# Kernel tuning notes

Hardware: AMD Instinct MI355X
Metric: run time of the kernel (lower is better)

Reference implementation:

```python
import jax, jax.numpy as jnp
import numpy as np

B, S, D, H = 4, 2048, 1024, 16
DK = D // H
NEG = -1e9


def setup_inputs() -> dict:
    key = jax.random.key(0)
    k1, k2, k3, k4 = jax.random.split(key, 4)
    x = jax.random.normal(k1, (B, S, D), dtype=jnp.float32)
    # seq_lens sorted descending; first entry must equal max_len (as the torch
    # code uses seq_lens[0] as max_len for the mask)
    sl = jax.random.randint(k2, (B,), S // 2, S + 1)
    sl = jnp.sort(sl)[::-1].at[0].set(S).astype(jnp.int64)
    # params of the output projection nn.Linear(d_m, d_m)
    lim = 1.0 / np.sqrt(D)
    W = jax.random.uniform(k3, (D, D), minval=-lim, maxval=lim, dtype=jnp.float32)
    b = jax.random.uniform(k4, (D,), minval=-lim, maxval=lim, dtype=jnp.float32)
    return {"x": x, "seq_lens": sl, "W": W, "b": b}


def reference(x, seq_lens, W, b):
    # key padding mask: (B, 1, 1, S) -> True where key position is valid
    valid = jnp.arange(S)[None, :] < seq_lens[:, None]          # (B, S)
    mask = valid[:, None, None, :]                              # (B, 1, 1, S)
    # split heads: (B, S, D) -> (B, H, S, DK)
    xh = x.reshape(B, S, H, DK).transpose(0, 2, 1, 3)
    scores = jnp.einsum("bhqd,bhkd->bhqk", xh, xh) / jnp.sqrt(jnp.float32(DK))
    scores = jnp.where(mask, scores, NEG)
    attn = jax.nn.softmax(scores, axis=-1)                      # (B, H, S, S)
    # dropout(0.1) omitted (eval-mode deterministic reference)
    ctx = jnp.einsum("bhqk,bhkd->bhqd", attn, xh)
    ctx = ctx.transpose(0, 2, 1, 3).reshape(B, S, D)
    out = ctx @ W.T + b                                         # (B, S, D)
    return (jnp.sum(out, axis=1), attn)
```

## Files before the change

### kernel.cpp

```cpp
#include <hip/hip_runtime.h>

#define S_  2048
#define D_  1024
#define H_  16
#define B_  4

typedef __attribute__((ext_vector_type(8))) short short8;
typedef __attribute__((ext_vector_type(4))) float f32x4;

__device__ __forceinline__ unsigned short f2bf(float f) {
  unsigned int u = __float_as_uint(f);
  u += 0x7fffu + ((u >> 16) & 1u);
  return (unsigned short)(u >> 16);
}
__device__ __forceinline__ unsigned int pack2(float a, float b) {
  return (unsigned int)f2bf(a) | ((unsigned int)f2bf(b) << 16);
}
__device__ __forceinline__ float h2f(unsigned int u, int shft) {
  unsigned short hs = (unsigned short)(u >> shft);
  return (float)__builtin_bit_cast(_Float16, hs);
}

#define SCL   0.18033688011112042f
#define EBIAS 12.0f

__global__ __launch_bounds__(256) void xcvt(const float* __restrict__ x,
                                            unsigned short* __restrict__ xh) {
  const int n = blockIdx.x;
  const int bh = n >> 5, chunk = n & 31;
  const int b = bh >> 4, h = bh & 15;
  const int r = threadIdx.x >> 2, cg = threadIdx.x & 3;
  const int srow = chunk * 64 + r;
  const float* src = x + ((size_t)b * S_ + srow) * D_ + h * 64 + cg * 16;
  float4 v0 = ((const float4*)src)[0];
  float4 v1 = ((const float4*)src)[1];
  float4 v2 = ((const float4*)src)[2];
  float4 v3 = ((const float4*)src)[3];
  uint4 w0, w1;
  w0.x = pack2(v0.x, v0.y); w0.y = pack2(v0.z, v0.w);
  w0.z = pack2(v1.x, v1.y); w0.w = pack2(v1.z, v1.w);
  w1.x = pack2(v2.x, v2.y); w1.y = pack2(v2.z, v2.w);
  w1.z = pack2(v3.x, v3.y); w1.w = pack2(v3.z, v3.w);
  unsigned short* dst = xh + ((size_t)bh * S_ + srow) * 64 + cg * 16;
  *(uint4*)dst = w0;
  *(uint4*)(dst + 8) = w1;
}

__global__ __launch_bounds__(256, 2) void attn_fused(
    const unsigned short* __restrict__ xh, const int* __restrict__ sl32,
    float* __restrict__ attn, unsigned int* __restrict__ cpart)
{
  __shared__ __align__(16) unsigned short kbuf[64 * 64];
  __shared__ __align__(16) unsigned int ebuf[8][2048];
  __shared__ float wbuf[4][16];
  __shared__ float invbuf[16];

  const int n    = blockIdx.x;
  const int xcd  = n & 7;
  const int slot = n >> 3;
  const int bh   = (slot >> 7) * 8 + xcd;
  const int qt   = slot & 127;
  const int b    = bh >> 4;
  const int tid  = threadIdx.x;
  const int wv   = tid >> 6;
  const int lane = tid & 63;
  const int lo   = lane & 15;
  const int g    = lane >> 4;

  const bool is64 = (sl32[1] == 0);
  const int seqlen = is64 ? sl32[2 * b] : sl32[b];

  const unsigned short* xk = xh + (size_t)bh * S_ * 64;

  short8 aq0 = *(const short8*)(xk + (size_t)(qt * 16 + lo) * 64 + g * 8);
  short8 aq1 = *(const short8*)(xk + (size_t)(qt * 16 + lo) * 64 + g * 8 + 32);

  const int sr = tid >> 2, up = tid & 3;
  uint4 pf0, pf1;
  auto prefetch = [&](int c) {
    const uint4* src = (const uint4*)(xk + (size_t)(c * 64 + sr) * 64) + up * 2;
    pf0 = src[0]; pf1 = src[1];
  };
  auto commit = [&]() {
    uint4* d = (uint4*)&kbuf[sr * 64];
    const int sw = sr & 7;
    d[(up * 2) ^ sw]     = pf0;
    d[(up * 2 + 1) ^ sw] = pf1;
  };

  float rsum[4] = {0.f, 0.f, 0.f, 0.f};
  prefetch(0);
  commit();
  __syncthreads();
  const int lk = wv * 16 + lo;
  const int cs = g ^ (lk & 7);
  const int sA = ((g * 2) & 6) << 2;
  for (int c = 0; c < 32; ++c) {
    if (c < 31) prefetch(c + 1);
    short8 b0 = *(const short8*)&kbuf[lk * 64 + cs * 8];
    short8 b1 = *(const short8*)&kbuf[lk * 64 + (cs ^ 4) * 8];
    f32x4 acc = {0.f, 0.f, 0.f, 0.f};
    acc = __builtin_amdgcn_mfma_f32_16x16x32_bf16(aq0, b0, acc, 0, 0, 0);
    acc = __builtin_amdgcn_mfma_f32_16x16x32_bf16(aq1, b1, acc, 0, 0, 0);
    const int kg = c * 64 + lk;
    const bool valid = kg < seqlen;
    float e0 = valid ? exp2f(acc[0] * SCL - EBIAS) : 0.f;
    float e1 = valid ? exp2f(acc[1] * SCL - EBIAS) : 0.f;
    float e2 = valid ? exp2f(acc[2] * SCL - EBIAS) : 0.f;
    float e3 = valid ? exp2f(acc[3] * SCL - EBIAS) : 0.f;
    rsum[0] += e0; rsum[1] += e1; rsum[2] += e2; rsum[3] += e3;
    ebuf[g * 2][kg ^ sA] =
        __builtin_bit_cast(unsigned int, __builtin_amdgcn_cvt_pkrtz(e0, e1));
    ebuf[g * 2 + 1][kg ^ sA] =
        __builtin_bit_cast(unsigned int, __builtin_amdgcn_cvt_pkrtz(e2, e3));
    __syncthreads();
    if (c < 31) commit();
    __syncthreads();
  }

#pragma unroll
  for (int r = 0; r < 4; ++r) {
    float v = rsum[r];
    v += __shfl_xor(v, 1);
    v += __shfl_xor(v, 2);
    v += __shfl_xor(v, 4);
    v += __shfl_xor(v, 8);
    if (lo == 0) wbuf[wv][g * 4 + r] = v;
  }
  __syncthreads();
  if (tid < 16)
    invbuf[tid] = 1.0f / (wbuf[0][tid] + wbuf[1][tid] + wbuf[2][tid] + wbuf[3][tid]);
  __syncthreads();

  const int wr = tid >> 4, wc = tid & 15;
  const int r2w = wr >> 1, shw = (wr & 1) * 16, sw2 = (r2w & 6) << 2;
  const float vr = invbuf[wr];
  float* prow = attn + (size_t)bh * S_ * S_ + (size_t)(qt * 16 + wr) * S_;
#pragma unroll 8
  for (int i = 0; i < 32; ++i) {
    const int k0 = wc * 4 + i * 64;
    uint4 u = *(const uint4*)&ebuf[r2w][k0 ^ sw2];
    f32x4 v = {h2f(u.x, shw) * vr, h2f(u.y, shw) * vr,
               h2f(u.z, shw) * vr, h2f(u.w, shw) * vr};
    __builtin_nontemporal_store(v, (f32x4*)(prow + k0));
  }

  const int c0 = tid * 8;
  float a0 = 0.f, a1 = 0.f, a2 = 0.f, a3 = 0.f;
  float a4 = 0.f, a5 = 0.f, a6 = 0.f, a7 = 0.f;
#pragma unroll
  for (int r2 = 0; r2 < 8; ++r2) {
    const int s = (r2 & 6) << 2;
    const uint4 uA = *(const uint4*)&ebuf[r2][c0 ^ s];
    const uint4 uB = *(const uint4*)&ebuf[r2][(c0 ^ s) + 4];
    const float i0 = invbuf[2 * r2], i1 = invbuf[2 * r2 + 1];
    a0 += h2f(uA.x, 0) * i0 + h2f(uA.x, 16) * i1;
    a1 += h2f(uA.y, 0) * i0 + h2f(uA.y, 16) * i1;
    a2 += h2f(uA.z, 0) * i0 + h2f(uA.z, 16) * i1;
    a3 += h2f(uA.w, 0) * i0 + h2f(uA.w, 16) * i1;
    a4 += h2f(uB.x, 0) * i0 + h2f(uB.x, 16) * i1;
    a5 += h2f(uB.y, 0) * i0 + h2f(uB.y, 16) * i1;
    a6 += h2f(uB.z, 0) * i0 + h2f(uB.z, 16) * i1;
    a7 += h2f(uB.w, 0) * i0 + h2f(uB.w, 16) * i1;
  }
  uint4 w;
  w.x = __builtin_bit_cast(unsigned int, __builtin_amdgcn_cvt_pkrtz(a0, a1));
  w.y = __builtin_bit_cast(unsigned int, __builtin_amdgcn_cvt_pkrtz(a2, a3));
  w.z = __builtin_bit_cast(unsigned int, __builtin_amdgcn_cvt_pkrtz(a4, a5));
  w.w = __builtin_bit_cast(unsigned int, __builtin_amdgcn_cvt_pkrtz(a6, a7));
  *(uint4*)&cpart[(size_t)(bh * 128 + qt) * 1024 + tid * 4] = w;
}

__global__ __launch_bounds__(256) void creduce(const unsigned int* __restrict__ cpart,
                                               float* __restrict__ c) {
  const int i = blockIdx.x * 256 + threadIdx.x;
  const int bh = i >> 11, k = i & 2047;
  const unsigned short* cp = (const unsigned short*)cpart + (size_t)bh * 128 * 2048 + k;
  float s = 0.f;
#pragma unroll 8
  for (int qt = 0; qt < 128; ++qt)
    s += (float)__builtin_bit_cast(_Float16, cp[(size_t)qt * 2048]);
  c[i] = s;
}

__global__ __launch_bounds__(256) void csum_k(const float* __restrict__ c,
                                              const unsigned short* __restrict__ xh,
                                              float* __restrict__ csump) {
  __shared__ float part[4][64];
  const int bh = blockIdx.x >> 3, oct = blockIdx.x & 7;
  const int seg = threadIdx.x >> 6, d = threadIdx.x & 63;
  const float* cb = c + bh * 2048;
  const unsigned short* xb = xh + (size_t)bh * S_ * 64 + d;
  const int k0 = oct * 256 + seg * 64;
  float acc = 0.f;
#pragma unroll 4
  for (int k = k0; k < k0 + 64; ++k) {
    float xv = __uint_as_float((unsigned int)xb[(size_t)k * 64] << 16);
    acc += cb[k] * xv;
  }
  part[seg][d] = acc;
  __syncthreads();
  if (threadIdx.x < 64)
    csump[((size_t)oct * 64 + bh) * 64 + d] =
        part[0][d] + part[1][d] + part[2][d] + part[3][d];
}

__global__ __launch_bounds__(256) void proj_k(const float* __restrict__ csump,
                                              const float* __restrict__ W,
                                              const float* __restrict__ bias,
                                              float* __restrict__ out0) {
  const int idx = blockIdx.x * 4 + (threadIdx.x >> 6);
  const int b = idx >> 10, d = idx & 1023;
  const int lane = threadIdx.x & 63;
  const float* wr = W + (size_t)d * D_;
  float acc = 0.f;
#pragma unroll
  for (int e = 0; e < 16; ++e) {
    const int ei = lane + e * 64;
    const int bhh = b * 16 + (ei >> 6);
    const int dd = ei & 63;
    float cv = 0.f;
#pragma unroll
    for (int oct = 0; oct < 8; ++oct)
      cv += csump[((size_t)oct * 64 + bhh) * 64 + dd];
    acc += cv * wr[ei];
  }
  acc += __shfl_xor(acc, 32);
  acc += __shfl_xor(acc, 16);
  acc += __shfl_xor(acc, 8);
  acc += __shfl_xor(acc, 4);
  acc += __shfl_xor(acc, 2);
  acc += __shfl_xor(acc, 1);
  if (lane == 0) out0[idx] = acc + 2048.0f * bias[d];
}

extern "C" void kernel_launch(void* const* d_in, const int* in_sizes, int n_in,
                              void* d_out, int out_size, void* d_ws, size_t ws_size,
                              hipStream_t stream) {
  const float* x    = (const float*)d_in[0];
  const int*   sl   = (const int*)d_in[1];
  const float* W    = (const float*)d_in[2];
  const float* bias = (const float*)d_in[3];

  float* out0 = (float*)d_out;
  float* attn = out0 + B_ * D_;

  unsigned int* cpart = (unsigned int*)d_ws;
  float* c     = (float*)(cpart + (size_t)64 * 128 * 1024);
  float* csump = c + 64 * 2048;
  unsigned short* xh = (unsigned short*)(csump + 8 * 64 * 64);

  hipLaunchKernelGGL(xcvt,       dim3(2048), dim3(256), 0, stream, x, xh);
  hipLaunchKernelGGL(attn_fused, dim3(8192), dim3(256), 0, stream, xh, sl, attn, cpart);
  hipLaunchKernelGGL(creduce,    dim3(512),  dim3(256), 0, stream, cpart, c);
  hipLaunchKernelGGL(csum_k,     dim3(512),  dim3(256), 0, stream, c, xh, csump);
  hipLaunchKernelGGL(proj_k,     dim3(1024), dim3(256), 0, stream, csump, W, bias, out0);
}
```

Baseline: 322.2 us.

## Double-buffer K tile to drop a barrier and fuse creduce into csum kernel

```diff
diff --git a/kernel.cpp b/kernel.cpp
--- a/kernel.cpp
+++ b/kernel.cpp
@@ -50,10 +50,10 @@
     const unsigned short* __restrict__ xh, const int* __restrict__ sl32,
     float* __restrict__ attn, unsigned int* __restrict__ cpart)
 {
-  __shared__ __align__(16) unsigned short kbuf[64 * 64];
+  __shared__ __align__(16) unsigned short kbuf[2][64 * 64];
   __shared__ __align__(16) unsigned int ebuf[8][2048];
-  __shared__ float wbuf[4][16];
-  __shared__ float invbuf[16];
+  float* wbuf   = (float*)&kbuf[0][0];
+  float* invbuf = (float*)&kbuf[1][0];
 
   const int n    = blockIdx.x;
   const int xcd  = n & 7;
@@ -81,8 +81,8 @@
     const uint4* src = (const uint4*)(xk + (size_t)(c * 64 + sr) * 64) + up * 2;
     pf0 = src[0]; pf1 = src[1];
   };
-  auto commit = [&]() {
-    uint4* d = (uint4*)&kbuf[sr * 64];
+  auto commit = [&](unsigned short* dst) {
+    uint4* d = (uint4*)&dst[sr * 64];
     const int sw = sr & 7;
     d[(up * 2) ^ sw]     = pf0;
     d[(up * 2 + 1) ^ sw] = pf1;
@@ -90,15 +90,16 @@
 
   float rsum[4] = {0.f, 0.f, 0.f, 0.f};
   prefetch(0);
-  commit();
+  commit(kbuf[0]);
   __syncthreads();
   const int lk = wv * 16 + lo;
   const int cs = g ^ (lk & 7);
   const int sA = ((g * 2) & 6) << 2;
   for (int c = 0; c < 32; ++c) {
     if (c < 31) prefetch(c + 1);
-    short8 b0 = *(const short8*)&kbuf[lk * 64 + cs * 8];
-    short8 b1 = *(const short8*)&kbuf[lk * 64 + (cs ^ 4) * 8];
+    const unsigned short* kb = kbuf[c & 1];
+    short8 b0 = *(const short8*)&kb[lk * 64 + cs * 8];
+    short8 b1 = *(const short8*)&kb[lk * 64 + (cs ^ 4) * 8];
     f32x4 acc = {0.f, 0.f, 0.f, 0.f};
     acc = __builtin_amdgcn_mfma_f32_16x16x32_bf16(aq0, b0, acc, 0, 0, 0);
     acc = __builtin_amdgcn_mfma_f32_16x16x32_bf16(aq1, b1, acc, 0, 0, 0);
@@ -113,8 +114,7 @@
         __builtin_bit_cast(unsigned int, __builtin_amdgcn_cvt_pkrtz(e0, e1));
     ebuf[g * 2 + 1][kg ^ sA] =
         __builtin_bit_cast(unsigned int, __builtin_amdgcn_cvt_pkrtz(e2, e3));
-    __syncthreads();
-    if (c < 31) commit();
+    if (c < 31) commit(kbuf[(c + 1) & 1]);
     __syncthreads();
   }
 
@@ -125,11 +125,11 @@
     v += __shfl_xor(v, 2);
     v += __shfl_xor(v, 4);
     v += __shfl_xor(v, 8);
-    if (lo == 0) wbuf[wv][g * 4 + r] = v;
+    if (lo == 0) wbuf[wv * 16 + g * 4 + r] = v;
   }
   __syncthreads();
   if (tid < 16)
-    invbuf[tid] = 1.0f / (wbuf[0][tid] + wbuf[1][tid] + wbuf[2][tid] + wbuf[3][tid]);
+    invbuf[tid] = 1.0f / (wbuf[tid] + wbuf[16 + tid] + wbuf[32 + tid] + wbuf[48 + tid]);
   __syncthreads();
 
   const int wr = tid >> 4, wc = tid & 15;
@@ -171,36 +171,36 @@
   *(uint4*)&cpart[(size_t)(bh * 128 + qt) * 1024 + tid * 4] = w;
 }
 
-__global__ __launch_bounds__(256) void creduce(const unsigned int* __restrict__ cpart,
-                                               float* __restrict__ c) {
-  const int i = blockIdx.x * 256 + threadIdx.x;
-  const int bh = i >> 11, k = i & 2047;
-  const unsigned short* cp = (const unsigned short*)cpart + (size_t)bh * 128 * 2048 + k;
-  float s = 0.f;
-#pragma unroll 8
-  for (int qt = 0; qt < 128; ++qt)
-    s += (float)__builtin_bit_cast(_Float16, cp[(size_t)qt * 2048]);
-  c[i] = s;
-}
-
-__global__ __launch_bounds__(256) void csum_k(const float* __restrict__ c,
-                                              const unsigned short* __restrict__ xh,
-                                              float* __restrict__ csump) {
+__global__ __launch_bounds__(256) void csum2(const unsigned int* __restrict__ cpart,
+                                             const unsigned short* __restrict__ xh,
+                                             float* __restrict__ csump) {
+  __shared__ float csh[256];
   __shared__ float part[4][64];
   const int bh = blockIdx.x >> 3, oct = blockIdx.x & 7;
-  const int seg = threadIdx.x >> 6, d = threadIdx.x & 63;
-  const float* cb = c + bh * 2048;
+  const int t = threadIdx.x;
+  {
+    const int k = oct * 256 + t;
+    const unsigned short* cp =
+        (const unsigned short*)cpart + (size_t)bh * 128 * 2048 + k;
+    float s = 0.f;
+#pragma unroll 8
+    for (int q = 0; q < 128; ++q)
+      s += (float)__builtin_bit_cast(_Float16, cp[(size_t)q * 2048]);
+    csh[t] = s;
+  }
+  __syncthreads();
+  const int seg = t >> 6, d = t & 63;
   const unsigned short* xb = xh + (size_t)bh * S_ * 64 + d;
   const int k0 = oct * 256 + seg * 64;
   float acc = 0.f;
 #pragma unroll 4
-  for (int k = k0; k < k0 + 64; ++k) {
-    float xv = __uint_as_float((unsigned int)xb[(size_t)k * 64] << 16);
-    acc += cb[k] * xv;
+  for (int kk = 0; kk < 64; ++kk) {
+    float xv = __uint_as_float((unsigned int)xb[(size_t)(k0 + kk) * 64] << 16);
+    acc += csh[seg * 64 + kk] * xv;
   }
   part[seg][d] = acc;
   __syncthreads();
-  if (threadIdx.x < 64)
+  if (t < 64)
     csump[((size_t)oct * 64 + bh) * 64 + d] =
         part[0][d] + part[1][d] + part[2][d] + part[3][d];
 }
@@ -246,13 +246,11 @@
   float* attn = out0 + B_ * D_;
 
   unsigned int* cpart = (unsigned int*)d_ws;
-  float* c     = (float*)(cpart + (size_t)64 * 128 * 1024);
-  float* csump = c + 64 * 2048;
+  float* csump = (float*)(cpart + (size_t)64 * 128 * 1024);
   unsigned short* xh = (unsigned short*)(csump + 8 * 64 * 64);
 
   hipLaunchKernelGGL(xcvt,       dim3(2048), dim3(256), 0, stream, x, xh);
   hipLaunchKernelGGL(attn_fused, dim3(8192), dim3(256), 0, stream, xh, sl, attn, cpart);
-  hipLaunchKernelGGL(creduce,    dim3(512),  dim3(256), 0, stream, cpart, c);
-  hipLaunchKernelGGL(csum_k,     dim3(512),  dim3(256), 0, stream, c, xh, csump);
+  hipLaunchKernelGGL(csum2,      dim3(512),  dim3(256), 0, stream, cpart, xh, csump);
   hipLaunchKernelGGL(proj_k,     dim3(1024), dim3(256), 0, stream, csump, W, bias, out0);
 }
```

Result: faster. 309.4 us (-4.0%).
